# Kernel tuning notes

Hardware: AMD Instinct MI355X
Metric: run time of the kernel (lower is better)

Reference implementation:

```python
import jax, jax.numpy as jnp
import numpy as np

B, N, D = 2, 2048, 1024
H = 16
HD = D // H  # 64
N_CTX = 256


def setup_inputs() -> dict:
    key = jax.random.key(0)
    ks = jax.random.split(key, 10)
    x = jax.random.normal(ks[0], (B, N, D), dtype=jnp.float32)
    ctx_ppr = jax.random.uniform(ks[1], (N_CTX,), dtype=jnp.float32, minval=1e-4, maxval=1.0)
    ctx_trust = jax.random.uniform(ks[2], (N_CTX,), dtype=jnp.float32)
    attn_mask = jax.random.randint(ks[3], (N, N), 0, 2).astype(jnp.bool_)
    # parameters (nn.Linear convention: y = x @ W.T + b)
    s_in = 1.0 / np.sqrt(D)
    W_in = jax.random.uniform(ks[4], (3 * D, D), dtype=jnp.float32, minval=-s_in, maxval=s_in)
    b_in = jax.random.uniform(ks[5], (3 * D,), dtype=jnp.float32, minval=-s_in, maxval=s_in)
    W_out = jax.random.uniform(ks[6], (D, D), dtype=jnp.float32, minval=-s_in, maxval=s_in)
    b_out = jax.random.uniform(ks[7], (D,), dtype=jnp.float32, minval=-s_in, maxval=s_in)
    log_ppr_alpha = jnp.ones((1,), jnp.float32) * 0.1
    trust_scale = jnp.ones((1,), jnp.float32) * 0.1
    return {"x": x, "ctx_ppr": ctx_ppr, "ctx_trust": ctx_trust, "n_ctx": N_CTX,
            "attn_mask": attn_mask, "W_in": W_in, "b_in": b_in,
            "W_out": W_out, "b_out": b_out,
            "log_ppr_alpha": log_ppr_alpha, "trust_scale": trust_scale}


def reference(x, ctx_ppr, ctx_trust, n_ctx, attn_mask, W_in, b_in, W_out, b_out,
              log_ppr_alpha, trust_scale):
    Bx, Nx, Dx = x.shape
    scale = HD ** -0.5
    qkv = x @ W_in.T + b_in  # [B,N,3D]
    q, k, v = jnp.split(qkv, 3, axis=-1)
    q = q.reshape(Bx, Nx, H, HD).transpose(0, 2, 1, 3)  # [B,H,N,d]
    k = k.reshape(Bx, Nx, H, HD).transpose(0, 2, 1, 3)
    v = v.reshape(Bx, Nx, H, HD).transpose(0, 2, 1, 3)
    if n_ctx > 0:
        gate = jax.nn.sigmoid(trust_scale[0] * ctx_trust)  # [n_ctx]
        gate_full = jnp.concatenate([gate, jnp.ones(Nx - n_ctx, x.dtype)])
        v = v * gate_full[None, None, :, None]
    logits = jnp.einsum('bhqd,bhkd->bhqk', q, k) * scale
    if n_ctx > 0:
        bias = log_ppr_alpha[0] * jnp.log(jnp.clip(ctx_ppr, 1e-8, None))
        col_bias = jnp.concatenate([bias, jnp.zeros(Nx - n_ctx, x.dtype)])
        logits = logits + col_bias[None, None, None, :]
    logits = jnp.where(attn_mask[None, None, :, :], -jnp.inf, logits)
    weights = jax.nn.softmax(logits, axis=-1)
    out = jnp.einsum('bhqk,bhkd->bhqd', weights, v)
    out = out.transpose(0, 2, 1, 3).reshape(Bx, Nx, Dx)
    return out @ W_out.T + b_out
```

## Files before the change

### kernel.cpp

```cpp
#include <hip/hip_runtime.h>
#include <hip/hip_bf16.h>
#include <math.h>

#define B_   2
#define N_   2048
#define D_   1024
#define H_   16
#define TD_  3072
#define LOG2E 1.44269504088896340736f
#define SCALE_Q (0.125f * LOG2E)

typedef short  bf16x8 __attribute__((ext_vector_type(8)));
typedef _Float16 f16x8 __attribute__((ext_vector_type(8)));
typedef _Float16 f16x4 __attribute__((ext_vector_type(4)));
typedef float  f32x4  __attribute__((ext_vector_type(4)));
typedef float  f32x16 __attribute__((ext_vector_type(16)));

#define MFMA16(a, b, c)   __builtin_amdgcn_mfma_f32_16x16x32_bf16(a, b, c, 0, 0, 0)
#define MFMA32B(a, b, c)  __builtin_amdgcn_mfma_f32_32x32x16_bf16(a, b, c, 0, 0, 0)
#define MFMA32H(a, b, c)  __builtin_amdgcn_mfma_f32_32x32x16_f16(a, b, c, 0, 0, 0)

__device__ __forceinline__ ushort f2bf(float f) {
    union { float f; unsigned u; } v; v.f = f;
    unsigned r = (v.u + 0x7fffu + ((v.u >> 16) & 1u)) >> 16;
    return (ushort)r;
}
__device__ __forceinline__ unsigned pkrtz(float a, float b) {
    typedef __fp16 h2 __attribute__((ext_vector_type(2)));
    union { h2 h; unsigned u; } c;
    c.h = __builtin_amdgcn_cvt_pkrtz(a, b);
    return c.u;
}
__device__ __forceinline__ void async16(const void* g, void* l) {
    __builtin_amdgcn_global_load_lds(
        (const __attribute__((address_space(1))) unsigned*)g,
        (__attribute__((address_space(3))) unsigned*)l, 16, 0, 0);
}
__device__ __forceinline__ void plswap(unsigned &a, unsigned &b) {
    auto r = __builtin_amdgcn_permlane32_swap((int)a, (int)b, false, false);
    a = (unsigned)r[0]; b = (unsigned)r[1];
}

__global__ __launch_bounds__(256) void preprocess(
    const float* __restrict__ x, const float* __restrict__ W_in,
    const float* __restrict__ W_out, const float* __restrict__ ctx_ppr,
    const float* __restrict__ log_alpha, const int* __restrict__ n_ctx_p,
    const int* __restrict__ mask,
    ushort* __restrict__ xb, ushort* __restrict__ wib, ushort* __restrict__ wob,
    float* __restrict__ biasrow, unsigned* __restrict__ maskbits)
{
    const int J0 = 1048576, J1 = 786432, J2 = 262144, JM = 131072, JB = 2048;
    int t = blockIdx.x * 256 + threadIdx.x;
    if (t < J0 + J1 + J2) {
        const float* src; ushort* dst; int i = t;
        if (i < J0)           { src = x;      dst = xb;  }
        else if (i < J0 + J1) { i -= J0;      src = W_in;  dst = wib; }
        else                  { i -= J0 + J1; src = W_out; dst = wob; }
        float4 v = ((const float4*)src)[i];
        ushort4 o;
        o.x = f2bf(v.x); o.y = f2bf(v.y); o.z = f2bf(v.z); o.w = f2bf(v.w);
        ((ushort4*)dst)[i] = o;
    } else if (t < J0 + J1 + J2 + JM) {
        int i = t - (J0 + J1 + J2);
        const int4* m = (const int4*)(mask + (size_t)i * 32);
        unsigned bits = 0u;
        #pragma unroll
        for (int j = 0; j < 8; ++j) {
            int4 w = m[j];
            bits |= (w.x != 0 ? 1u : 0u) << (j * 4 + 0);
            bits |= (w.y != 0 ? 1u : 0u) << (j * 4 + 1);
            bits |= (w.z != 0 ? 1u : 0u) << (j * 4 + 2);
            bits |= (w.w != 0 ? 1u : 0u) << (j * 4 + 3);
        }
        maskbits[i] = bits;
    } else if (t < J0 + J1 + J2 + JM + JB) {
        int k = t - (J0 + J1 + J2 + JM);
        int nc = n_ctx_p[0];
        float bv = 0.f;
        if (k < nc) bv = log_alpha[0] * __log2f(fmaxf(ctx_ppr[k], 1e-8f));
        biasrow[k] = bv;
    }
}

template<int BCOL, int MODE>
__global__ __launch_bounds__(256) void gemm_bt(
    const ushort* __restrict__ A, const ushort* __restrict__ Bw,
    const float* __restrict__ bias, float* __restrict__ Cout,
    ushort* __restrict__ qkout, _Float16* __restrict__ vTout,
    int Ncol, int K,
    const float* __restrict__ ctx_trust, const float* __restrict__ trust_scale,
    const int* __restrict__ n_ctx_p)
{
    constexpr int NT = BCOL / 32;
    __shared__ ushort tA[128 * 64];
    __shared__ ushort tB[BCOL * 64];
    const int tid = threadIdx.x;
    const int lane = tid & 63, wv = tid >> 6;
    const int ln = lane & 15, kg = lane >> 4;
    const int rh = wv >> 1, ch = wv & 1;
    const int row0 = blockIdx.y * 128, col0 = blockIdx.x * BCOL;

    int offA[2][4], offB[2][NT];
    #pragma unroll
    for (int kk = 0; kk < 2; ++kk) {
        #pragma unroll
        for (int i = 0; i < 4; ++i) {
            int ra = rh * 64 + i * 16 + ln;
            offA[kk][i] = ra * 64 + (((kk * 4 + kg) ^ (ra & 7)) << 3);
        }
        #pragma unroll
        for (int i = 0; i < NT; ++i) {
            int rb = ch * (BCOL / 2) + i * 16 + ln;
            offB[kk][i] = rb * 64 + (((kk * 4 + kg) ^ (rb & 7)) << 3);
        }
    }
    f32x4 acc[4][NT];
    #pragma unroll
    for (int i = 0; i < 4; ++i)
        #pragma unroll
        for (int j = 0; j < NT; ++j) acc[i][j] = (f32x4){0.f, 0.f, 0.f, 0.f};

    for (int kt = 0; kt < K; kt += 64) {
        __syncthreads();
        #pragma unroll
        for (int r2 = 0; r2 < 4; ++r2) {
            int g = r2 * 256 + tid, row = g >> 3, sg = (g & 7) ^ (row & 7);
            async16(A + (size_t)(row0 + row) * K + kt + sg * 8, &tA[g * 8]);
        }
        #pragma unroll
        for (int r2 = 0; r2 < BCOL / 32; ++r2) {
            int g = r2 * 256 + tid, row = g >> 3, sg = (g & 7) ^ (row & 7);
            async16(Bw + (size_t)(col0 + row) * K + kt + sg * 8, &tB[g * 8]);
        }
        __syncthreads();
        #pragma unroll
        for (int kk = 0; kk < 2; ++kk) {
            bf16x8 af[4], bfr[NT];
            #pragma unroll
            for (int i = 0; i < 4; ++i)  af[i]  = *(const bf16x8*)&tA[offA[kk][i]];
            #pragma unroll
            for (int i = 0; i < NT; ++i) bfr[i] = *(const bf16x8*)&tB[offB[kk][i]];
            #pragma unroll
            for (int mt = 0; mt < 4; ++mt)
                #pragma unroll
                for (int nt = 0; nt < NT; ++nt)
                    acc[mt][nt] = MFMA16(af[mt], bfr[nt], acc[mt][nt]);
        }
    }

    const int nctx = n_ctx_p ? n_ctx_p[0] : 0;
    const float ts = trust_scale ? trust_scale[0] : 0.f;
    #pragma unroll
    for (int nt = 0; nt < NT; ++nt) {
        int col = col0 + ch * (BCOL / 2) + nt * 16 + ln;
        float bv = bias[col];
        #pragma unroll
        for (int mt = 0; mt < 4; ++mt) {
            int rbase = row0 + rh * 64 + mt * 16 + kg * 4;
            f32x4 a = acc[mt][nt];
            if (MODE == 0) {
                #pragma unroll
                for (int reg = 0; reg < 4; ++reg)
                    Cout[(size_t)(rbase + reg) * Ncol + col] = a[reg] + bv;
            } else {
                if (col < D_) {
                    #pragma unroll
                    for (int reg = 0; reg < 4; ++reg)
                        qkout[(size_t)(rbase + reg) * 2048 + col] =
                            f2bf((a[reg] + bv) * SCALE_Q);
                } else if (col < 2 * D_) {
                    #pragma unroll
                    for (int reg = 0; reg < 4; ++reg)
                        qkout[(size_t)(rbase + reg) * 2048 + col] = f2bf(a[reg] + bv);
                } else {
                    int vc = col - 2 * D_;
                    int hh = vc >> 6, dim = vc & 63;
                    int bb = rbase >> 11, nbase = rbase & (N_ - 1);
                    ushort4 o;
                    #pragma unroll
                    for (int reg = 0; reg < 4; ++reg) {
                        float v = a[reg] + bv;
                        int n = nbase + reg;
                        if (n < nctx) {
                            float g = 1.f / (1.f + __expf(-ts * ctx_trust[n]));
                            v *= g;
                        }
                        _Float16 hv = (_Float16)v;
                        ((ushort*)&o)[reg] = *(ushort*)&hv;
                    }
                    *(ushort4*)&vTout[((size_t)(bb * 16 + hh) * 64 + dim) * 2048 + nbase] = o;
                }
            }
        }
    }
}

__global__ __launch_bounds__(256, 4) void attn(
    const ushort* __restrict__ qkb,
    const _Float16* __restrict__ vT,
    const unsigned* __restrict__ maskbits,
    const float* __restrict__ biasrow,
    const int* __restrict__ n_ctx_p,
    _Float16* __restrict__ op0,
    _Float16* __restrict__ op1,
    float* __restrict__ lpart)
{
    __shared__ ushort   Kt[3][64 * 64];
    __shared__ _Float16 Vt[2][64 * 64];
    const int tid = threadIdx.x;
    const int lane = tid & 63, wv = tid >> 6;
    const int q31 = lane & 31, hi = lane >> 5;
    const int b = blockIdx.y >> 4, h = blockIdx.y & 15;
    const int q0w = blockIdx.x * 128 + wv * 32;
    const int kh = blockIdx.z;
    const int kbase = kh << 10;
    const int nctx = n_ctx_p[0];

    const int lin = blockIdx.x + (blockIdx.y << 4) + (blockIdx.z << 9);
    const int rot = ((lin >> 8) << 2) & 15;

    union fi { float f; int i; };
    fi ng; ng.f = -1e30f;
    const int NEGI = ng.i;

    bf16x8 qf[4];
    {
        const ushort* qrow = qkb + (size_t)(b * N_ + q0w + q31) * 2048 + h * 64;
        #pragma unroll
        for (int ks = 0; ks < 4; ++ks)
            qf[ks] = *(const bf16x8*)(qrow + ks * 16 + hi * 8);
    }
    const size_t kgbase = (size_t)(b * N_ + kbase) * 2048 + 1024 + h * 64;
    const _Float16* vbase = vT + (size_t)((b * 16 + h) * 64) * 2048 + kbase;
    const unsigned* mrow = maskbits + (size_t)(q0w + q31) * 64 + (kbase >> 5);

    int goff[2], ldso[2];
    #pragma unroll
    for (int r2 = 0; r2 < 2; ++r2) {
        int g = r2 * 256 + tid, row = g >> 3, sg = (g & 7) ^ (row & 7);
        goff[r2] = row * 2048 + sg * 8;
        ldso[r2] = g * 8;
    }

    f32x16 O[2];
    O[0] = (f32x16)(0.f); O[1] = (f32x16)(0.f);
    float lrun = 0.f;

    const int cp0 = rot, cp1 = (rot + 1) & 15;
    uint2 mcur = *(const uint2*)&mrow[cp0 * 2];
    asm volatile("" ::: "memory");
    {
        const ushort* gp0 = qkb + kgbase + (size_t)cp0 * (64 * 2048);
        #pragma unroll
        for (int r2 = 0; r2 < 2; ++r2) async16(gp0 + goff[r2], &Kt[0][ldso[r2]]);
        const _Float16* vp = vbase + cp0 * 64;
        #pragma unroll
        for (int r2 = 0; r2 < 2; ++r2) async16(vp + goff[r2], &Vt[0][ldso[r2]]);
        const ushort* gp1 = qkb + kgbase + (size_t)cp1 * (64 * 2048);
        #pragma unroll
        for (int r2 = 0; r2 < 2; ++r2) async16(gp1 + goff[r2], &Kt[1][ldso[r2]]);
    }

    const int swz = q31 & 7;
    int kb = 0;
    #pragma unroll 1
    for (int ci = 0; ci < 16; ++ci) {
        asm volatile("s_barrier" ::: "memory");
        uint2 mnext = mcur;
        if (ci < 15) {
            const int cpv = (ci + 1 + rot) & 15;
            mnext = *(const uint2*)&mrow[cpv * 2];
            asm volatile("" ::: "memory");
            const _Float16* vp = vbase + cpv * 64;
            #pragma unroll
            for (int r2 = 0; r2 < 2; ++r2)
                async16(vp + goff[r2], &Vt[(ci + 1) & 1][ldso[r2]]);
        }
        if (ci < 14) {
            int nb = kb + 2; if (nb >= 3) nb -= 3;
            const int cpk = (ci + 2 + rot) & 15;
            const ushort* gp = qkb + kgbase + (size_t)cpk * (64 * 2048);
            #pragma unroll
            for (int r2 = 0; r2 < 2; ++r2)
                async16(gp + goff[r2], &Kt[nb][ldso[r2]]);
        }
        if (ci < 14)       asm volatile("s_waitcnt vmcnt(7)" ::: "memory");
        else if (ci == 14) asm volatile("s_waitcnt vmcnt(5)" ::: "memory");
        else               asm volatile("s_waitcnt vmcnt(0)" ::: "memory");
        asm volatile("s_barrier" ::: "memory");

        const ushort*   KT = Kt[kb];
        const _Float16* VT = Vt[ci & 1];
        const int cp = (ci + rot) & 15;
        const int c0g = kbase + cp * 64;
        const bool has_bias = (c0g < nctx);
        float lsum = 0.f;

        #pragma unroll
        for (int t = 0; t < 2; ++t) {
            f32x16 S = (f32x16)(0.f);
            const int rbase = (t * 32 + q31) * 64;
            __builtin_amdgcn_s_setprio(1);
            #pragma unroll
            for (int ks = 0; ks < 4; ++ks) {
                bf16x8 kf = *(const bf16x8*)&KT[rbase + (((ks * 2 + hi) ^ swz) << 3)];
                S = MFMA32B(kf, qf[ks], S);
            }
            __builtin_amdgcn_s_setprio(0);

            const unsigned msh = (t ? mcur.y : mcur.x) >> (hi * 4);
            unsigned pk[8];
            float lt = 0.f;
            #pragma unroll
            for (int g = 0; g < 4; ++g) {
                f32x4 bb;
                if (has_bias)
                    bb = *(const f32x4*)&biasrow[c0g + t * 32 + g * 8 + hi * 4];
                float pr[4];
                #pragma unroll
                for (int r = 0; r < 4; ++r) {
                    const int br = r + 8 * g;
                    float s = S[g * 4 + r];
                    if (has_bias) s += bb[r];
                    int mi = ((int)(msh << (31 - br))) >> 31;
                    fi su; su.f = s;
                    su.i = (mi & NEGI) | (su.i & ~mi);
                    pr[r] = __builtin_amdgcn_exp2f(su.f);
                }
                lt += (pr[0] + pr[1]) + (pr[2] + pr[3]);
                pk[g * 2 + 0] = pkrtz(pr[0], pr[1]);
                pk[g * 2 + 1] = pkrtz(pr[2], pr[3]);
            }
            lsum += lt;

            __builtin_amdgcn_s_setprio(1);
            #pragma unroll
            for (int kss = 0; kss < 2; ++kss) {
                const int ks = 2 * t + kss, lo4 = kss * 4;
                unsigned w0 = pk[lo4 + 0], w1 = pk[lo4 + 1];
                unsigned w2 = pk[lo4 + 2], w3 = pk[lo4 + 3];
                plswap(w0, w2);
                plswap(w1, w3);
                union { f16x8 v; unsigned u[4]; } frag;
                frag.u[0] = w0; frag.u[1] = w1;
                frag.u[2] = w2; frag.u[3] = w3;
                #pragma unroll
                for (int t2 = 0; t2 < 2; ++t2) {
                    const int vb = (t2 * 32 + q31) * 64;
                    union { f16x8 v; int4 i4; } vf;
                    vf.i4 = *(const int4*)&VT[vb + (((ks * 2 + hi) ^ swz) << 3)];
                    O[t2] = MFMA32H(vf.v, frag.v, O[t2]);
                }
            }
            __builtin_amdgcn_s_setprio(0);
        }
        lrun += lsum;
        mcur = mnext;
        kb = kb + 1; if (kb >= 3) kb -= 3;
    }

    float l = lrun + __shfl_xor(lrun, 32);
    float inv = 1.f / l;
    _Float16* orow = (kh ? op1 : op0)
                   + (size_t)(b * N_ + q0w + q31) * 1024 + h * 64;
    #pragma unroll
    for (int t = 0; t < 2; ++t)
        #pragma unroll
        for (int g = 0; g < 4; ++g) {
            ushort4 o;
            #pragma unroll
            for (int r = 0; r < 4; ++r) {
                _Float16 hv = (_Float16)(O[t][g * 4 + r] * inv);
                ((ushort*)&o)[r] = *(ushort*)&hv;
            }
            *(ushort4*)&orow[t * 32 + g * 8 + hi * 4] = o;
        }
    if (hi == 0)
        lpart[(kh << 16) + (b * 16 + h) * 2048 + q0w + q31] = l;
}

__global__ __launch_bounds__(256) void combine(
    const _Float16* __restrict__ op0, const _Float16* __restrict__ op1,
    const float* __restrict__ lpart, ushort* __restrict__ attb)
{
    int t = blockIdx.x * 256 + threadIdx.x;
    size_t idx = (size_t)t * 4;
    int col = (int)(idx & 1023);
    int row = (int)(idx >> 10);
    int h = col >> 6;
    int b = row >> 11, q = row & 2047;
    int lidx = (b * 16 + h) * 2048 + q;
    float l0 = lpart[lidx], l1 = lpart[65536 + lidx];
    float inv = 1.f / (l0 + l1);
    float w0 = l0 * inv, w1 = l1 * inv;
    f16x4 a0 = *(const f16x4*)(op0 + idx);
    f16x4 a1 = *(const f16x4*)(op1 + idx);
    ushort4 o;
    #pragma unroll
    for (int r = 0; r < 4; ++r)
        ((ushort*)&o)[r] = f2bf((float)a0[r] * w0 + (float)a1[r] * w1);
    *(ushort4*)(attb + idx) = o;
}

extern "C" void kernel_launch(void* const* d_in, const int* in_sizes, int n_in,
                              void* d_out, int out_size, void* d_ws, size_t ws_size,
                              hipStream_t stream)
{
    const float* x         = (const float*)d_in[0];
    const float* ctx_ppr   = (const float*)d_in[1];
    const float* ctx_trust = (const float*)d_in[2];
    const int*   n_ctx_p   = (const int*)d_in[3];
    const int*   attn_mask = (const int*)d_in[4];
    const float* W_in      = (const float*)d_in[5];
    const float* b_in      = (const float*)d_in[6];
    const float* W_out     = (const float*)d_in[7];
    const float* b_out     = (const float*)d_in[8];
    const float* log_alpha = (const float*)d_in[9];
    const float* trust_sc  = (const float*)d_in[10];
    float* out = (float*)d_out;

    char* ws = (char*)d_ws;
    ushort*    xb       = (ushort*)ws;    ws += (size_t)4096 * 1024 * 2;
    ushort*    wib      = (ushort*)ws;    ws += (size_t)3072 * 1024 * 2;
    ushort*    wob      = (ushort*)ws;    ws += (size_t)1024 * 1024 * 2;
    ushort*    qkb      = (ushort*)ws;    ws += (size_t)4096 * 2048 * 2;
    _Float16*  vT       = (_Float16*)ws;  ws += (size_t)2048 * 2048 * 2;
    ushort*    attbuf   = (ushort*)ws;    ws += (size_t)4096 * 1024 * 2;
    float*     biasrow  = (float*)ws;     ws += 2048 * 4;
    unsigned*  maskbits = (unsigned*)ws;  ws += (size_t)2048 * 64 * 4;

    _Float16* op0   = (_Float16*)xb;
    _Float16* op1   = (_Float16*)attbuf;
    float*    lpart = (float*)wib;

    hipLaunchKernelGGL(preprocess, dim3(8712), dim3(256), 0, stream,
                       x, W_in, W_out, ctx_ppr, log_alpha, n_ctx_p, attn_mask,
                       xb, wib, wob, biasrow, maskbits);

    hipLaunchKernelGGL((gemm_bt<128, 1>), dim3(24, 32), dim3(256), 0, stream,
                       xb, wib, b_in, (float*)nullptr, qkb, vT, TD_, 1024,
                       ctx_trust, trust_sc, n_ctx_p);

    hipLaunchKernelGGL(attn, dim3(16, 32, 2), dim3(256), 0, stream,
                       qkb, vT, maskbits, biasrow, n_ctx_p, op0, op1, lpart);

    hipLaunchKernelGGL(combine, dim3(4096), dim3(256), 0, stream,
                       op0, op1, lpart, attbuf);

    hipLaunchKernelGGL((gemm_bt<64, 0>), dim3(16, 32), dim3(256), 0, stream,
                       attbuf, wob, b_out, out, (ushort*)nullptr, (_Float16*)nullptr,
                       1024, 1024, ctx_trust, trust_sc, n_ctx_p);
}
```

Baseline: 245.9 us.

## Rewrite GEMMs with 32x32 MFMA, double-buffered LDS, and XCD-aware block mapping

Replaces the single-buffered 16x16x32 MFMA GEMM with a 32x32x16 MFMA variant. It double-buffers the LDS tiles so the next K-tile's async loads overlap compute, using explicit s_barrier and vmcnt waits. It also remaps a 1D grid so consecutive blocks spread across the XCDs, and widens the QKV GEMM tile to 192 columns so the grid is 512 blocks. The cost is more LDS, hand-tuned wait counts that must match the number of issued loads, and a more complex epilogue layout.

Measured after the change: 248.2 us. Within noise of the previous version (+0.9%).

```diff
diff --git a/kernel.cpp b/kernel.cpp
--- a/kernel.cpp
+++ b/kernel.cpp
@@ -16,7 +16,6 @@
 typedef float  f32x4  __attribute__((ext_vector_type(4)));
 typedef float  f32x16 __attribute__((ext_vector_type(16)));
 
-#define MFMA16(a, b, c)   __builtin_amdgcn_mfma_f32_16x16x32_bf16(a, b, c, 0, 0, 0)
 #define MFMA32B(a, b, c)  __builtin_amdgcn_mfma_f32_32x32x16_bf16(a, b, c, 0, 0, 0)
 #define MFMA32H(a, b, c)  __builtin_amdgcn_mfma_f32_32x32x16_f16(a, b, c, 0, 0, 0)
 
@@ -83,7 +82,7 @@
 }
 
 template<int BCOL, int MODE>
-__global__ __launch_bounds__(256) void gemm_bt(
+__global__ __launch_bounds__(256) void gemm32(
     const ushort* __restrict__ A, const ushort* __restrict__ Bw,
     const float* __restrict__ bias, float* __restrict__ Cout,
     ushort* __restrict__ qkout, _Float16* __restrict__ vTout,
@@ -91,102 +90,142 @@
     const float* __restrict__ ctx_trust, const float* __restrict__ trust_scale,
     const int* __restrict__ n_ctx_p)
 {
-    constexpr int NT = BCOL / 32;
-    __shared__ ushort tA[128 * 64];
-    __shared__ ushort tB[BCOL * 64];
+    constexpr int CT = BCOL / 64;
+    constexpr int LB = BCOL / 32;
+    __shared__ ushort tA[2][128 * 64];
+    __shared__ ushort tB[2][BCOL * 64];
     const int tid = threadIdx.x;
     const int lane = tid & 63, wv = tid >> 6;
-    const int ln = lane & 15, kg = lane >> 4;
+    const int q31 = lane & 31, hi = lane >> 5;
     const int rh = wv >> 1, ch = wv & 1;
-    const int row0 = blockIdx.y * 128, col0 = blockIdx.x * BCOL;
-
-    int offA[2][4], offB[2][NT];
-    #pragma unroll
-    for (int kk = 0; kk < 2; ++kk) {
-        #pragma unroll
-        for (int i = 0; i < 4; ++i) {
-            int ra = rh * 64 + i * 16 + ln;
-            offA[kk][i] = ra * 64 + (((kk * 4 + kg) ^ (ra & 7)) << 3);
-        }
-        #pragma unroll
-        for (int i = 0; i < NT; ++i) {
-            int rb = ch * (BCOL / 2) + i * 16 + ln;
-            offB[kk][i] = rb * 64 + (((kk * 4 + kg) ^ (rb & 7)) << 3);
-        }
-    }
-    f32x4 acc[4][NT];
-    #pragma unroll
-    for (int i = 0; i < 4; ++i)
-        #pragma unroll
-        for (int j = 0; j < NT; ++j) acc[i][j] = (f32x4){0.f, 0.f, 0.f, 0.f};
-
-    for (int kt = 0; kt < K; kt += 64) {
-        __syncthreads();
-        #pragma unroll
-        for (int r2 = 0; r2 < 4; ++r2) {
-            int g = r2 * 256 + tid, row = g >> 3, sg = (g & 7) ^ (row & 7);
-            async16(A + (size_t)(row0 + row) * K + kt + sg * 8, &tA[g * 8]);
-        }
-        #pragma unroll
-        for (int r2 = 0; r2 < BCOL / 32; ++r2) {
-            int g = r2 * 256 + tid, row = g >> 3, sg = (g & 7) ^ (row & 7);
-            async16(Bw + (size_t)(col0 + row) * K + kt + sg * 8, &tB[g * 8]);
-        }
-        __syncthreads();
-        #pragma unroll
-        for (int kk = 0; kk < 2; ++kk) {
-            bf16x8 af[4], bfr[NT];
-            #pragma unroll
-            for (int i = 0; i < 4; ++i)  af[i]  = *(const bf16x8*)&tA[offA[kk][i]];
-            #pragma unroll
-            for (int i = 0; i < NT; ++i) bfr[i] = *(const bf16x8*)&tB[offB[kk][i]];
-            #pragma unroll
-            for (int mt = 0; mt < 4; ++mt)
-                #pragma unroll
-                for (int nt = 0; nt < NT; ++nt)
-                    acc[mt][nt] = MFMA16(af[mt], bfr[nt], acc[mt][nt]);
-        }
+    const int id = blockIdx.x;
+    const int wg = (id & 7) * 64 + (id >> 3);
+    const int row0 = (wg >> 4) * 128, col0 = (wg & 15) * BCOL;
+
+    const int swz = q31 & 7;
+    int offAr[2], offBr[CT];
+    #pragma unroll
+    for (int rt = 0; rt < 2; ++rt) offAr[rt] = (rh * 64 + rt * 32 + q31) * 64;
+    #pragma unroll
+    for (int ct = 0; ct < CT; ++ct) offBr[ct] = (ch * (BCOL / 2) + ct * 32 + q31) * 64;
+
+    f32x16 acc[2][CT];
+    #pragma unroll
+    for (int i = 0; i < 2; ++i)
+        #pragma unroll
+        for (int j = 0; j < CT; ++j) acc[i][j] = (f32x16)(0.f);
+
+    int arow[4], asg[4], brow[LB], bsg[LB];
+    #pragma unroll
+    for (int r2 = 0; r2 < 4; ++r2) {
+        int g = r2 * 256 + tid;
+        arow[r2] = g >> 3; asg[r2] = ((g & 7) ^ ((g >> 3) & 7)) << 3;
+    }
+    #pragma unroll
+    for (int r2 = 0; r2 < LB; ++r2) {
+        int g = r2 * 256 + tid;
+        brow[r2] = g >> 3; bsg[r2] = ((g & 7) ^ ((g >> 3) & 7)) << 3;
+    }
+    const ushort* Ab = A + (size_t)row0 * K;
+    const ushort* Bb = Bw + (size_t)col0 * K;
+
+    auto issue = [&](int ktile, int bufi) {
+        const int kt = ktile * 64;
+        #pragma unroll
+        for (int r2 = 0; r2 < 4; ++r2)
+            async16(Ab + (size_t)arow[r2] * K + kt + asg[r2],
+                    &tA[bufi][(r2 * 256 + tid) * 8]);
+        #pragma unroll
+        for (int r2 = 0; r2 < LB; ++r2)
+            async16(Bb + (size_t)brow[r2] * K + kt + bsg[r2],
+                    &tB[bufi][(r2 * 256 + tid) * 8]);
+    };
+
+    issue(0, 0);
+    const int NIT = K / 64;
+    #pragma unroll 1
+    for (int it = 0; it < NIT; ++it) {
+        const int cur = it & 1;
+        asm volatile("s_barrier" ::: "memory");
+        if (it + 1 < NIT) {
+            issue(it + 1, cur ^ 1);
+            if constexpr (BCOL == 192)
+                asm volatile("s_waitcnt vmcnt(10)" ::: "memory");
+            else
+                asm volatile("s_waitcnt vmcnt(6)" ::: "memory");
+        } else {
+            asm volatile("s_waitcnt vmcnt(0)" ::: "memory");
+        }
+        asm volatile("s_barrier" ::: "memory");
+
+        const ushort* KA = tA[cur];
+        const ushort* KB = tB[cur];
+        __builtin_amdgcn_s_setprio(1);
+        #pragma unroll
+        for (int kk = 0; kk < 4; ++kk) {
+            const int gr = ((kk * 2 + hi) ^ swz) << 3;
+            bf16x8 af[2], bfv[CT];
+            #pragma unroll
+            for (int rt = 0; rt < 2; ++rt)
+                af[rt] = *(const bf16x8*)&KA[offAr[rt] + gr];
+            #pragma unroll
+            for (int ct = 0; ct < CT; ++ct)
+                bfv[ct] = *(const bf16x8*)&KB[offBr[ct] + gr];
+            #pragma unroll
+            for (int rt = 0; rt < 2; ++rt)
+                #pragma unroll
+                for (int ct = 0; ct < CT; ++ct)
+                    acc[rt][ct] = MFMA32B(af[rt], bfv[ct], acc[rt][ct]);
+        }
+        __builtin_amdgcn_s_setprio(0);
     }
 
     const int nctx = n_ctx_p ? n_ctx_p[0] : 0;
     const float ts = trust_scale ? trust_scale[0] : 0.f;
     #pragma unroll
-    for (int nt = 0; nt < NT; ++nt) {
-        int col = col0 + ch * (BCOL / 2) + nt * 16 + ln;
-        float bv = bias[col];
-        #pragma unroll
-        for (int mt = 0; mt < 4; ++mt) {
-            int rbase = row0 + rh * 64 + mt * 16 + kg * 4;
-            f32x4 a = acc[mt][nt];
+    for (int ct = 0; ct < CT; ++ct) {
+        const int col = col0 + ch * (BCOL / 2) + ct * 32 + q31;
+        const float bv = bias[col];
+        #pragma unroll
+        for (int rt = 0; rt < 2; ++rt) {
+            const int rb0 = row0 + rh * 64 + rt * 32 + 4 * hi;
+            f32x16 a = acc[rt][ct];
             if (MODE == 0) {
                 #pragma unroll
-                for (int reg = 0; reg < 4; ++reg)
-                    Cout[(size_t)(rbase + reg) * Ncol + col] = a[reg] + bv;
+                for (int g2 = 0; g2 < 4; ++g2)
+                    #pragma unroll
+                    for (int r = 0; r < 4; ++r)
+                        Cout[(size_t)(rb0 + 8 * g2 + r) * Ncol + col] = a[g2 * 4 + r] + bv;
+            } else if (col < D_) {
+                #pragma unroll
+                for (int g2 = 0; g2 < 4; ++g2)
+                    #pragma unroll
+                    for (int r = 0; r < 4; ++r)
+                        qkout[(size_t)(rb0 + 8 * g2 + r) * 2048 + col] =
+                            f2bf((a[g2 * 4 + r] + bv) * SCALE_Q);
+            } else if (col < 2 * D_) {
+                #pragma unroll
+                for (int g2 = 0; g2 < 4; ++g2)
+                    #pragma unroll
+                    for (int r = 0; r < 4; ++r)
+                        qkout[(size_t)(rb0 + 8 * g2 + r) * 2048 + col] =
+                            f2bf(a[g2 * 4 + r] + bv);
             } else {
-                if (col < D_) {
-                    #pragma unroll
-                    for (int reg = 0; reg < 4; ++reg)
-                        qkout[(size_t)(rbase + reg) * 2048 + col] =
-                            f2bf((a[reg] + bv) * SCALE_Q);
-                } else if (col < 2 * D_) {
-                    #pragma unroll
-                    for (int reg = 0; reg < 4; ++reg)
-                        qkout[(size_t)(rbase + reg) * 2048 + col] = f2bf(a[reg] + bv);
-                } else {
-                    int vc = col - 2 * D_;
-                    int hh = vc >> 6, dim = vc & 63;
-                    int bb = rbase >> 11, nbase = rbase & (N_ - 1);
+                const int vc = col - 2 * D_;
+                const int hh = vc >> 6, dim = vc & 63;
+                const int bb = row0 >> 11;
+                #pragma unroll
+                for (int g2 = 0; g2 < 4; ++g2) {
+                    const int nbase = (rb0 + 8 * g2) & (N_ - 1);
                     ushort4 o;
                     #pragma unroll
-                    for (int reg = 0; reg < 4; ++reg) {
-                        float v = a[reg] + bv;
-                        int n = nbase + reg;
-                        if (n < nctx) {
-                            float g = 1.f / (1.f + __expf(-ts * ctx_trust[n]));
-                            v *= g;
-                        }
+                    for (int r = 0; r < 4; ++r) {
+                        float v = a[g2 * 4 + r] + bv;
+                        const int n = nbase + r;
+                        if (n < nctx)
+                            v *= 1.f / (1.f + __expf(-ts * ctx_trust[n]));
                         _Float16 hv = (_Float16)v;
-                        ((ushort*)&o)[reg] = *(ushort*)&hv;
+                        ((ushort*)&o)[r] = *(ushort*)&hv;
                     }
                     *(ushort4*)&vTout[((size_t)(bb * 16 + hh) * 64 + dim) * 2048 + nbase] = o;
                 }
@@ -437,7 +476,7 @@
                        x, W_in, W_out, ctx_ppr, log_alpha, n_ctx_p, attn_mask,
                        xb, wib, wob, biasrow, maskbits);
 
-    hipLaunchKernelGGL((gemm_bt<128, 1>), dim3(24, 32), dim3(256), 0, stream,
+    hipLaunchKernelGGL((gemm32<192, 1>), dim3(512), dim3(256), 0, stream,
                        xb, wib, b_in, (float*)nullptr, qkb, vT, TD_, 1024,
                        ctx_trust, trust_sc, n_ctx_p);
 
@@ -447,7 +486,7 @@
     hipLaunchKernelGGL(combine, dim3(4096), dim3(256), 0, stream,
                        op0, op1, lpart, attbuf);
 
-    hipLaunchKernelGGL((gemm_bt<64, 0>), dim3(16, 32), dim3(256), 0, stream,
+    hipLaunchKernelGGL((gemm32<64, 0>), dim3(512), dim3(256), 0, stream,
                        attbuf, wob, b_out, out, (ushort*)nullptr, (_Float16*)nullptr,
                        1024, 1024, ctx_trust, trust_sc, n_ctx_p);
 }
```
